# Kernel tuning notes

Measured on AMD Instinct MI355X. Metric: run time of the kernel, lower is better.

The kernel has to match this reference:

```python
import jax, jax.numpy as jnp
import numpy as np

# SLAYER neuron / simulation constants (from params)
THETA = 10.0      # spike threshold
TAU_SR = 10.0     # PSP (synaptic response) time constant
TS = 1.0          # simulation time step
TAU_RHO = 1.0     # surrogate-gradient width
SCALE_RHO = 1.0   # surrogate-gradient scale
ALPHA = float(np.exp(-TS / TAU_SR))  # leaky-filter decay per step

B, C_IN, T = 32, 156, 2048
HID, OUT = 512, 20


@jax.custom_vjp
def spike(u):
    # Hard threshold with SLAYER-style exponential surrogate gradient.
    return (u >= THETA).astype(u.dtype)

def _spike_fwd(u):
    return spike(u), u

def _spike_bwd(u, g):
    sg = (SCALE_RHO / TAU_RHO) * jnp.exp(-jnp.abs(u - THETA) / TAU_RHO)
    return (g * sg,)

spike.defvjp(_spike_fwd, _spike_bwd)


def psp(x):
    # Leaky exponential temporal filter along the LAST axis (SLAYER psp):
    # y[t] = ALPHA * y[t-1] + x[t]
    xt = jnp.moveaxis(x, -1, 0)  # [T, ...]
    def step(c, xi):
        c = ALPHA * c + xi
        return c, c
    _, y = jax.lax.scan(step, jnp.zeros_like(xt[0]), xt)
    return jnp.moveaxis(y, 0, -1)


def dense(x, W):
    # SLAYER dense layer: per-timestep fully-connected over channel dim.
    # x: [N, C, H, W, T], W: [O, C] -> [N, O, H, W, T]
    return jnp.einsum('oc,nchwt->nohwt', W, x)


def _make_perm():
    rng = np.random.default_rng(0)
    random_list = rng.permutation(np.arange(1, 40))
    perm = []
    for i in random_list:
        perm.append(2 * int(i) - 2)
        perm.append(2 * int(i) - 1)
    for i in random_list:
        perm.append(2 * int(i) - 2 + 78)
        perm.append(2 * int(i) - 1 + 78)
    return jnp.asarray(perm, dtype=jnp.int32)


def setup_inputs() -> dict:
    key = jax.random.key(0)
    k0, k1, k2, k3, k4 = jax.random.split(key, 5)
    spike_input = jax.random.randint(k0, (B, C_IN, 1, 1, T), 0, 2).astype(jnp.float32)
    W1 = jax.random.normal(k1, (HID, C_IN), dtype=jnp.float32) * (C_IN ** -0.5)
    W2 = jax.random.normal(k2, (OUT, HID), dtype=jnp.float32) * (HID ** -0.5)
    Wl1 = jax.random.normal(k3, (HID, T), dtype=jnp.float32) * (T ** -0.5)
    Wl2 = jax.random.normal(k4, (OUT, HID), dtype=jnp.float32) * (HID ** -0.5)
    perm = _make_perm()
    return {"spike_input": spike_input, "W1": W1, "W2": W2,
            "Wl1": Wl1, "Wl2": Wl2, "perm": perm}


def reference(spike_input, W1, W2, Wl1, Wl2, perm):
    # Branch 1: channel-dense over taxels, PSP + spike, twice.
    s1 = spike(psp(dense(spike_input, W1)))          # [B, HID, 1, 1, T]
    spike_output = spike(psp(dense(s1, W2)))         # [B, OUT, 1, 1, T]

    # Branch 2: transpose channel<->time, permute taxel axis, dense over time dim.
    x_t = jnp.swapaxes(spike_input, 1, 4)            # [B, T, 1, 1, C_IN]
    x_tp = x_t[..., perm]                            # gather on taxel axis
    l1 = spike(psp(dense(x_tp, Wl1)))                # [B, HID, 1, 1, C_IN]
    location_output = spike(psp(dense(l1, Wl2)))     # [B, OUT, 1, 1, C_IN]

    return jnp.concatenate([spike_output, location_output], axis=4)
```

## Files before the change

### kernel.cpp

```cpp
#include <hip/hip_runtime.h>

#define ALPHA  0.90483741803595952f
#define ALPHA8 0.44932896411722156f
#define THETA  10.0f
#define BF1    ((unsigned short)0x3F80)
#define ISCALE 0.015625f

typedef short   bf16x8 __attribute__((ext_vector_type(8)));
typedef float   f32x4  __attribute__((ext_vector_type(4)));
typedef float   f32x4v __attribute__((ext_vector_type(4)));
typedef unsigned short ushort4v __attribute__((ext_vector_type(4)));
typedef unsigned short ushort8v __attribute__((ext_vector_type(8)));
typedef unsigned char  uchar4v  __attribute__((ext_vector_type(4)));
typedef unsigned char  uchar8v  __attribute__((ext_vector_type(8)));
typedef long long i64;

#define DMA16(gsrc, ldst)                                                     \
    __builtin_amdgcn_global_load_lds(                                         \
        (const __attribute__((address_space(1))) unsigned int*)(gsrc),        \
        (__attribute__((address_space(3))) unsigned int*)(ldst), 16, 0, 0)

__device__ __forceinline__ unsigned short f2bf(float f) {
    unsigned int x = __float_as_uint(f);
    unsigned int r = (x + 0x7FFFu + ((x >> 16) & 1u)) >> 16;
    return (unsigned short)r;
}
__device__ __forceinline__ float bf2f(unsigned short h) {
    return __uint_as_float(((unsigned int)h) << 16);
}
__device__ __forceinline__ void split2(float w, unsigned short& h0,
                                       unsigned short& h1) {
    h0 = f2bf(w);          float r0 = w - bf2f(h0);
    h1 = f2bf(r0);
}
__device__ __forceinline__ unsigned char f2fp8(float f) {
    int pk = __builtin_amdgcn_cvt_pk_fp8_f32(f, 0.f, 0, false);
    return (unsigned char)(pk & 0xFF);
}
__device__ __forceinline__ float fp82f(unsigned char b) {
    return __builtin_amdgcn_cvt_f32_fp8((int)b, 0);
}

__global__ __launch_bounds__(256) void prep_scan_pack(
    const float* __restrict__ In, unsigned char* __restrict__ Infp8,
    unsigned short* __restrict__ Pbf,
    const float* __restrict__ W1,  const float* __restrict__ W2,
    const float* __restrict__ Wl1, const float* __restrict__ Wl2,
    unsigned short* __restrict__ W1p,  unsigned char* __restrict__ W2p8,
    unsigned char* __restrict__ Wl1p8, unsigned short* __restrict__ Wl2p)
{
    const int blk = blockIdx.x;
    if (blk >= 4992) {
        const int bidx = blk - 4992;
        if (bidx >= 512 && bidx < 544) {
            int m = bidx - 512;
            for (int k = threadIdx.x; k < 512; k += 256) {
                float w = (m < 20) ? W2[(long long)m * 512 + k] : 0.f;
                unsigned char h0 = f2fp8(w);
                unsigned char h1 = f2fp8(w - fp82f(h0));
                W2p8[(long long)m * 512 + k] = h0;
                W2p8[16384 + (long long)m * 512 + k] = h1;
            }
        } else if (bidx >= 544 && bidx < 1056) {
            int m = bidx - 544;
            for (int k = threadIdx.x; k < 2048; k += 256) {
                float w = Wl1[(long long)m * 2048 + k] * 64.0f;
                unsigned char h0 = f2fp8(w);
                unsigned char h1 = f2fp8(w - fp82f(h0));
                Wl1p8[(long long)m * 2048 + k] = h0;
                Wl1p8[1048576 + (long long)m * 2048 + k] = h1;
            }
        } else {
            const float* W; unsigned short* P; int M, K, Kp, Mp, m;
            if (bidx < 512) { W = W1;  P = W1p;  M = 512; K = 156; Kp = 160; Mp = 512; m = bidx; }
            else            { W = Wl2; P = Wl2p; M = 20;  K = 512; Kp = 512; Mp = 32;  m = bidx - 1056; }
            for (int k = threadIdx.x; k < Kp; k += 256) {
                float v = (m < M && k < K) ? W[(long long)m * K + k] : 0.f;
                unsigned short h0, h1;
                split2(v, h0, h1);
                P[(long long)m * Kp + k] = h0;
                P[(long long)Mp * Kp + (long long)m * Kp + k] = h1;
            }
        }
        return;
    }

    const int row = blk;
    const int tid = threadIdx.x;
    const float* x = In + (long long)row * 2048 + tid * 8;
    const unsigned char ONE8 = f2fp8(1.0f);

    float v[8];
    *(f32x4v*)&v[0] = *(const f32x4v*)x;
    *(f32x4v*)&v[4] = *(const f32x4v*)(x + 4);

    uchar8v raw;
    #pragma unroll
    for (int k = 0; k < 8; ++k) raw[k] = (v[k] >= 0.5f) ? ONE8 : (unsigned char)0;
    *(uchar8v*)(Infp8 + (long long)row * 2048 + tid * 8) = raw;

    float y = 0.f;
    #pragma unroll
    for (int k = 0; k < 8; ++k) { y = ALPHA * y + v[k]; v[k] = y; }

    __shared__ float sc[256];
    float val = y;
    sc[tid] = val;
    float m = ALPHA8;
    for (int d = 1; d < 256; d <<= 1) {
        __syncthreads();
        float p = (tid >= d) ? sc[tid - d] : 0.f;
        __syncthreads();
        val += m * p;
        sc[tid] = val;
        m *= m;
    }
    __syncthreads();
    float carry = (tid > 0) ? sc[tid - 1] : 0.f;

    ushort8v pv;
    float ak = ALPHA;
    #pragma unroll
    for (int k = 0; k < 8; ++k) {
        float yk = v[k] + ak * carry;
        ak *= ALPHA;
        pv[k] = f2bf(yk);
    }
    *(ushort8v*)(Pbf + (long long)row * 2048 + tid * 8) = pv;
}

__global__ __launch_bounds__(256) void transposeP(
    const unsigned short* __restrict__ Pbf, unsigned short* __restrict__ PT)
{
    __shared__ unsigned short Tile[64][72];
    const int t0 = blockIdx.x * 64;
    const int c0 = blockIdx.y * 64;
    const int b  = blockIdx.z;
    const int tid = threadIdx.x;

    #pragma unroll
    for (int s = 0; s < 2; ++s) {
        int id = tid + s * 256;
        int cc = id >> 3;
        int t8 = (id & 7) * 8;
        ushort8v v = {0,0,0,0,0,0,0,0};
        if (c0 + cc < 156)
            v = *(const ushort8v*)(Pbf + (long long)(b * 156 + c0 + cc) * 2048 + t0 + t8);
        *(ushort8v*)&Tile[cc][t8] = v;
    }
    __syncthreads();

    #pragma unroll
    for (int s = 0; s < 2; ++s) {
        int id = tid + s * 256;
        int t  = id >> 3;
        int c8 = (id & 7) * 8;
        if (c0 + c8 + 7 < 160) {
            unsigned short r[8];
            #pragma unroll
            for (int j = 0; j < 8; ++j) r[j] = Tile[c8 + j][t];
            *(ushort8v*)(PT + (long long)b * 327680 + (long long)(t0 + t) * 160 + c0 + c8)
                = *(ushort8v*)r;
        }
    }
}

__global__ __launch_bounds__(256) void mega_gemm1(
    const unsigned short* __restrict__ W1p,
    const unsigned short* __restrict__ PT,
    unsigned short* __restrict__ S1bits,
    const unsigned char* __restrict__ Wl1p8,
    const unsigned char* __restrict__ Infp8,
    unsigned short* __restrict__ Zp)
{
    __shared__ alignas(16) unsigned char SMEM[49152];
    const int bx  = blockIdx.x;
    const int tid = threadIdx.x;
    const int lane = tid & 63, w = tid >> 6;
    const int wy = w >> 1, wx = w & 1;
    const int l15 = lane & 15, kq = lane >> 4;
    const int key = (l15 >> 1) & 3;

    if (bx >= 1280) {
        unsigned char* Ab = SMEM;
        unsigned char* Bb = SMEM + 32768;

        const int id1 = bx - 1280;
        const int z  = id1 >> 6;
        const int m0 = ((id1 >> 4) & 3) * 128;
        const int n0 = (id1 & 15) * 128;
        const unsigned short* Tb = PT + (long long)z * 327680;

        auto dmaA = [&](int buf, int k0) {
            #pragma unroll
            for (int s = 0; s < 4; ++s) {
                int id = tid + s * 256;
                int pl = id >> 9, m = (id >> 2) & 127, g = id & 3;
                int gs = g ^ ((m >> 1) & 3);
                DMA16(W1p + (long long)pl * 81920 +
                      (long long)(m0 + m) * 160 + k0 + gs * 8,
                      Ab + buf * 16384 + id * 16);
            }
        };
        auto dmaB = [&](int buf, int k0) {
            #pragma unroll
            for (int s = 0; s < 2; ++s) {
                int id = tid + s * 256;
                int n = id >> 2, g = id & 3;
                int gs = g ^ ((n >> 1) & 3);
                DMA16(Tb + (long long)(n0 + n) * 160 + k0 + gs * 8,
                      Bb + buf * 8192 + id * 16);
            }
        };

        int aOff[2][4], bOff[4];
        #pragma unroll
        for (int pl = 0; pl < 2; ++pl)
            #pragma unroll
            for (int mt = 0; mt < 4; ++mt)
                aOff[pl][mt] = pl * 8192 + (wy * 64 + mt * 16 + l15) * 64 +
                               ((kq ^ key) * 16);
        #pragma unroll
        for (int nt = 0; nt < 4; ++nt)
            bOff[nt] = (wx * 64 + nt * 16 + l15) * 64 + ((kq ^ key) * 16);

        f32x4 acc[4][4] = {};

        dmaA(0, 0); dmaB(0, 0);
        __syncthreads();

        #pragma unroll
        for (int it = 0; it < 5; ++it) {
            const int cur = it & 1;
            if (it < 4) { dmaA(cur ^ 1, (it + 1) * 32); dmaB(cur ^ 1, (it + 1) * 32); }

            const unsigned char* Ac = Ab + cur * 16384;
            const unsigned char* Bc = Bb + cur * 8192;
            bf16x8 bfr[4];
            #pragma unroll
            for (int nt = 0; nt < 4; ++nt)
                bfr[nt] = *(const bf16x8*)(Bc + bOff[nt]);
            #pragma unroll
            for (int pl = 0; pl < 2; ++pl) {
                #pragma unroll
                for (int mt = 0; mt < 4; ++mt) {
                    bf16x8 afr = *(const bf16x8*)(Ac + aOff[pl][mt]);
                    #pragma unroll
                    for (int nt = 0; nt < 4; ++nt)
                        acc[mt][nt] = __builtin_amdgcn_mfma_f32_16x16x32_bf16(
                            afr, bfr[nt], acc[mt][nt], 0, 0, 0);
                }
            }
            __syncthreads();
        }

        unsigned short* Db = S1bits + (long long)z * 512 * 128;
        #pragma unroll
        for (int mt = 0; mt < 4; ++mt) {
            #pragma unroll
            for (int i = 0; i < 4; ++i) {
                int m = m0 + wy * 64 + mt * 16 + kq * 4 + i;
                #pragma unroll
                for (int nt = 0; nt < 4; ++nt) {
                    unsigned long long mask = __ballot(acc[mt][nt][i] >= THETA);
                    if (l15 == 0) {
                        int nchunk = (n0 + wx * 64 + nt * 16) >> 4;
                        Db[(long long)m * 128 + nchunk] =
                            (unsigned short)((mask >> (kq * 16)) & 0xFFFFu);
                    }
                }
            }
        }
    } else {
        unsigned char* Ab = SMEM;
        unsigned char* Bb = SMEM + 16384;

        const int id0 = bx;
        const int nIdx = id0 % 40;
        if (nIdx >= 39) return;
        const int rest = id0 / 40;
        const int n0  = nIdx * 128;
        const int m0  = (rest & 7) * 64;
        const int ksl = rest >> 3;
        const int ks0 = ksl * 512;

        auto dmaA8 = [&](int buf, int kk) {
            #pragma unroll
            for (int s = 0; s < 2; ++s) {
                int id = tid + s * 256;
                int pl = id >> 8, m = (id >> 2) & 63, g = id & 3;
                int gs = g ^ ((m >> 1) & 3);
                DMA16(Wl1p8 + (long long)pl * 1048576 +
                      (long long)(m0 + m) * 2048 + kk + gs * 16,
                      Ab + buf * 8192 + id * 16);
            }
        };
        auto dmaB8 = [&](int buf, int kk) {
            #pragma unroll
            for (int s = 0; s < 2; ++s) {
                int id = tid + s * 256;
                int n = id >> 2, g = id & 3;
                int gs = g ^ ((n >> 1) & 3);
                DMA16(Infp8 + (long long)(n0 + n) * 2048 + kk + gs * 16,
                      Bb + buf * 8192 + id * 16);
            }
        };

        int aO8[2][2][2], bO8[4][2];
        #pragma unroll
        for (int ks = 0; ks < 2; ++ks) {
            const int gl = ks * 2 + (kq >> 1);
            const int sub = ((gl ^ key) * 16) + (kq & 1) * 8;
            #pragma unroll
            for (int pl = 0; pl < 2; ++pl)
                #pragma unroll
                for (int mt = 0; mt < 2; ++mt)
                    aO8[pl][mt][ks] = pl * 4096 +
                        (wy * 32 + mt * 16 + l15) * 64 + sub;
            #pragma unroll
            for (int nt = 0; nt < 4; ++nt)
                bO8[nt][ks] = (wx * 64 + nt * 16 + l15) * 64 + sub;
        }

        f32x4 acc[2][4] = {};

        dmaA8(0, ks0); dmaB8(0, ks0);
        __syncthreads();

        #pragma unroll
        for (int it = 0; it < 8; ++it) {
            const int cur = it & 1;
            if (it < 7) { dmaA8(cur ^ 1, ks0 + (it + 1) * 64);
                          dmaB8(cur ^ 1, ks0 + (it + 1) * 64); }

            const unsigned char* Ac = Ab + cur * 8192;
            const unsigned char* Bc = Bb + cur * 8192;
            #pragma unroll
            for (int ks = 0; ks < 2; ++ks) {
                i64 bfr[4];
                #pragma unroll
                for (int nt = 0; nt < 4; ++nt)
                    bfr[nt] = *(const i64*)(Bc + bO8[nt][ks]);
                #pragma unroll
                for (int pl = 0; pl < 2; ++pl) {
                    #pragma unroll
                    for (int mt = 0; mt < 2; ++mt) {
                        i64 afr = *(const i64*)(Ac + aO8[pl][mt][ks]);
                        #pragma unroll
                        for (int nt = 0; nt < 4; ++nt)
                            acc[mt][nt] = __builtin_amdgcn_mfma_f32_16x16x32_fp8_fp8(
                                afr, bfr[nt], acc[mt][nt], 0, 0, 0);
                    }
                }
            }
            __syncthreads();
        }

        unsigned short* Tu = (unsigned short*)SMEM;
        #pragma unroll
        for (int mt = 0; mt < 2; ++mt) {
            #pragma unroll
            for (int i = 0; i < 4; ++i) {
                int mL = wy * 32 + mt * 16 + kq * 4 + i;
                #pragma unroll
                for (int nt = 0; nt < 4; ++nt) {
                    int nL = wx * 64 + nt * 16 + l15;
                    Tu[mL * 129 + nL] = f2bf(acc[mt][nt][i] * ISCALE);
                }
            }
        }
        __syncthreads();

        unsigned short* Zs = Zp + (long long)ksl * 2555904;
        #pragma unroll
        for (int s2 = 0; s2 < 32; ++s2) {
            int id = tid + s2 * 256;
            int cL = id >> 6;
            int mL = id & 63;
            int n = n0 + cL;
            int bb = n / 156, cc = n - bb * 156;
            Zs[(long long)cc * 16384 + bb * 512 + m0 + mL] = Tu[mL * 129 + cL];
        }
    }
}

__global__ __launch_bounds__(256) void mega_stage2(
    const unsigned char* __restrict__ W2p8,
    const unsigned short* __restrict__ S1bits,
    float* __restrict__ C2p,
    const unsigned short* __restrict__ Zp,
    const int* __restrict__ perm,
    unsigned short* __restrict__ L1T)
{
    __shared__ alignas(16) unsigned char SMEM[20608];
    const int bx  = blockIdx.x;
    const int tid = threadIdx.x;

    if (bx < 1024) {
        auto As = (unsigned char (*)[32][72])SMEM;
        auto Bs = (unsigned char (*)[72])(SMEM + 4608);

        const int lane = tid & 63, w = tid >> 6;
        const int l15 = lane & 15, kq = lane >> 4;
        const int n0  = (bx & 15) * 128;
        const int ksl = (bx >> 4) & 1;
        const int b   = bx >> 5;
        const int ks0 = ksl * 256;

        const unsigned short* Bb = S1bits + (long long)b * 512 * 128;
        const unsigned char ONE8 = f2fp8(1.0f);

        int aPl[2], aM[2], aK8[2];
        #pragma unroll
        for (int s = 0; s < 2; ++s) {
            int id = tid + s * 256;
            aPl[s] = id >> 8; int rem = id & 255;
            aM[s] = rem >> 3; aK8[s] = (rem & 7) * 8;
        }
        const int kb = (tid >> 4) * 4;
        const int nb = (tid & 15) * 8;
        const int nchunk = (n0 + nb) >> 4;
        const int nshift = nb & 15;

        f32x4 acc[2][2] = {};
        uchar8v aReg[2];
        unsigned short bBits[4];

        auto loadA = [&](int k0) {
            #pragma unroll
            for (int s = 0; s < 2; ++s)
                aReg[s] = *(const uchar8v*)(W2p8 + (long long)aPl[s] * 16384 +
                                            (long long)aM[s] * 512 + k0 + aK8[s]);
        };
        auto loadB = [&](int k0) {
            #pragma unroll
            for (int kk2 = 0; kk2 < 4; ++kk2)
                bBits[kk2] = Bb[(long long)(k0 + kb + kk2) * 128 + nchunk];
        };
        auto stage = [&]() {
            #pragma unroll
            for (int s = 0; s < 2; ++s) *(uchar8v*)&As[aPl[s]][aM[s]][aK8[s]] = aReg[s];
            unsigned char bv[4][8];
            #pragma unroll
            for (int kk2 = 0; kk2 < 4; ++kk2) {
                unsigned int bits = ((unsigned int)bBits[kk2] >> nshift) & 0xFFu;
                #pragma unroll
                for (int j = 0; j < 8; ++j)
                    bv[kk2][j] = ((bits >> j) & 1u) ? ONE8 : (unsigned char)0;
            }
            #pragma unroll
            for (int j = 0; j < 8; ++j) {
                uchar4v v4 = { bv[0][j], bv[1][j], bv[2][j], bv[3][j] };
                *(uchar4v*)&Bs[nb + j][kb] = v4;
            }
        };

        loadA(ks0); loadB(ks0);
        stage();
        __syncthreads();

        #pragma unroll
        for (int it = 0; it < 4; ++it) {
            const int kn = ks0 + (it + 1) * 64;
            if (it < 3) { loadA(kn); loadB(kn); }

            #pragma unroll
            for (int ks = 0; ks < 2; ++ks) {
                i64 bfr[2];
                #pragma unroll
                for (int nt = 0; nt < 2; ++nt)
                    bfr[nt] = *(const i64*)&Bs[w * 32 + nt * 16 + l15][ks * 32 + kq * 8];
                #pragma unroll
                for (int s = 0; s < 2; ++s) {
                    #pragma unroll
                    for (int mt = 0; mt < 2; ++mt) {
                        i64 afr = *(const i64*)&As[s][mt * 16 + l15][ks * 32 + kq * 8];
                        #pragma unroll
                        for (int nt = 0; nt < 2; ++nt)
                            acc[mt][nt] = __builtin_amdgcn_mfma_f32_16x16x32_fp8_fp8(
                                afr, bfr[nt], acc[mt][nt], 0, 0, 0);
                    }
                }
            }
            __syncthreads();
            if (it < 3) {
                stage();
                __syncthreads();
            }
        }

        float* Cb = C2p + (long long)b * 20 * 2048 + (long long)ksl * 1310720LL;
        #pragma unroll
        for (int mt = 0; mt < 2; ++mt) {
            #pragma unroll
            for (int i = 0; i < 4; ++i) {
                int m = mt * 16 + kq * 4 + i;
                if (m >= 20) continue;
                #pragma unroll
                for (int nt = 0; nt < 2; ++nt) {
                    int n = n0 + w * 32 + nt * 16 + l15;
                    Cb[(long long)m * 2048 + n] = acc[mt][nt][i];
                }
            }
        }
    } else {
        auto Xs = (float (*)[32])SMEM;
        int* p  = (int*)(SMEM + 19968);

        const int r0 = (bx - 1024) * 32;
        for (int i = tid; i < 156; i += 256) p[i] = perm[i];

        const int row = tid & 31;
        const int cq  = tid >> 5;
        #pragma unroll
        for (int it = 0; it < 20; ++it) {
            int c = it * 8 + cq;
            if (c < 156) {
                long long base = (long long)c * 16384 + r0 + row;
                float s = bf2f(Zp[base]) + bf2f(Zp[base + 2555904]) +
                          bf2f(Zp[base + 2 * 2555904]) + bf2f(Zp[base + 3 * 2555904]);
                Xs[c][row] = s;
            }
        }
        __syncthreads();

        if (tid < 32) {
            float y = 0.f;
            for (int c = 0; c < 156; ++c) {
                y = ALPHA * y + Xs[p[c]][tid];
                L1T[(long long)c * 16384 + r0 + tid] = (y >= THETA) ? BF1 : 0;
            }
        }
    }
}

__global__ __launch_bounds__(256) void mega_stage3(
    const float* __restrict__ C2p, float* __restrict__ out,
    const unsigned short* __restrict__ Wl2p,
    const unsigned short* __restrict__ L1T)
{
    __shared__ alignas(16) unsigned char SMEM[36864];
    const int bx  = blockIdx.x;
    const int tid = threadIdx.x;

    if (bx < 640) {
        float* sc = (float*)SMEM;
        const int row = bx;
        const float* x = C2p + (long long)row * 2048 + tid * 8;

        float v[8];
        #pragma unroll
        for (int k = 0; k < 8; ++k) v[k] = x[k] + x[k + 1310720LL];

        float y = 0.f;
        #pragma unroll
        for (int k = 0; k < 8; ++k) { y = ALPHA * y + v[k]; v[k] = y; }

        float val = y;
        sc[tid] = val;
        float m = ALPHA8;
        for (int d = 1; d < 256; d <<= 1) {
            __syncthreads();
            float p = (tid >= d) ? sc[tid - d] : 0.f;
            __syncthreads();
            val += m * p;
            sc[tid] = val;
            m *= m;
        }
        __syncthreads();
        float carry = (tid > 0) ? sc[tid - 1] : 0.f;

        float* o = out + (long long)row * 2204 + tid * 8;
        float ak = ALPHA;
        #pragma unroll
        for (int k = 0; k < 8; ++k) {
            float yk = v[k] + ak * carry;
            ak *= ALPHA;
            o[k] = (yk >= THETA) ? 1.0f : 0.0f;
        }
    } else {
        auto As = (unsigned short (*)[32][72])SMEM;
        auto Bs = (unsigned short (*)[72])(SMEM + 9216);

        const int b  = bx - 640;
        const int lane = tid & 63, w = tid >> 6;
        const int l15 = lane & 15, kq = lane >> 4;

        f32x4 acc[2][3] = {};

        for (int k0 = 0; k0 < 512; k0 += 64) {
            #pragma unroll
            for (int s = 0; s < 2; ++s) {
                int id = tid + s * 256;
                int pl = id >> 8, rem = id & 255;
                int m = rem >> 3, k8 = (rem & 7) * 8;
                ushort8v v = *(const ushort8v*)(Wl2p + (long long)pl * 16384 +
                                                (long long)m * 512 + k0 + k8);
                *(ushort8v*)&As[pl][m][k8] = v;
            }
            #pragma unroll
            for (int s = 0; s < 6; ++s) {
                int id = tid + s * 256;
                int n = id >> 3, k8 = (id & 7) * 8;
                ushort8v v = {0,0,0,0,0,0,0,0};
                if (n < 156)
                    v = *(const ushort8v*)(L1T + (long long)n * 16384 +
                                           b * 512 + k0 + k8);
                *(ushort8v*)&Bs[n][k8] = v;
            }
            __syncthreads();

            #pragma unroll
            for (int ks = 0; ks < 2; ++ks) {
                bf16x8 bfr[3];
                #pragma unroll
                for (int nt = 0; nt < 3; ++nt)
                    bfr[nt] = *(const bf16x8*)&Bs[w * 48 + nt * 16 + l15][ks * 32 + kq * 8];
                #pragma unroll
                for (int s = 0; s < 2; ++s) {
                    #pragma unroll
                    for (int mt = 0; mt < 2; ++mt) {
                        bf16x8 afr = *(const bf16x8*)&As[s][mt * 16 + l15][ks * 32 + kq * 8];
                        #pragma unroll
                        for (int nt = 0; nt < 3; ++nt)
                            acc[mt][nt] = __builtin_amdgcn_mfma_f32_16x16x32_bf16(
                                afr, bfr[nt], acc[mt][nt], 0, 0, 0);
                    }
                }
            }
            __syncthreads();
        }

        float* Cs = (float*)SMEM;
        #pragma unroll
        for (int mt = 0; mt < 2; ++mt) {
            #pragma unroll
            for (int i = 0; i < 4; ++i) {
                int m = mt * 16 + kq * 4 + i;
                #pragma unroll
                for (int nt = 0; nt < 3; ++nt) {
                    int n = w * 48 + nt * 16 + l15;
                    Cs[m * 193 + n] = acc[mt][nt][i];
                }
            }
        }
        __syncthreads();

        if (tid < 20) {
            const float* cr = Cs + tid * 193;
            float* o = out + (long long)(b * 20 + tid) * 2204 + 2048;
            float y = 0.f;
            for (int c = 0; c < 156; ++c) {
                y = ALPHA * y + cr[c];
                o[c] = (y >= THETA) ? 1.0f : 0.0f;
            }
        }
    }
}

extern "C" void kernel_launch(void* const* d_in, const int* in_sizes, int n_in,
                              void* d_out, int out_size, void* d_ws, size_t ws_size,
                              hipStream_t stream)
{
    const float* In  = (const float*)d_in[0];
    const float* W1  = (const float*)d_in[1];
    const float* W2  = (const float*)d_in[2];
    const float* Wl1 = (const float*)d_in[3];
    const float* Wl2 = (const float*)d_in[4];
    const int*  perm = (const int*)d_in[5];
    float* out = (float*)d_out;

    float* ws = (float*)d_ws;
    unsigned short* S1bits = (unsigned short*)ws;
    float* C2p = ws + 1048576LL;
    unsigned char*  Infp8 = (unsigned char*)(ws + 3670016LL);
    unsigned short* Pbf  = (unsigned short*)(ws + 6225920LL);
    unsigned short* PT   = (unsigned short*)(ws + 11337728LL);
    unsigned short* W1p  = (unsigned short*)(ws + 16580608LL);
    unsigned char*  W2p8 = (unsigned char*)(ws + 16662528LL);
    unsigned char*  Wl1p8= (unsigned char*)(ws + 16670720LL);
    unsigned short* Wl2p = (unsigned short*)(ws + 17195008LL);
    unsigned short* Zpbf = (unsigned short*)(ws + 17211392LL);
    unsigned short* L1T  = (unsigned short*)(ws + 22323200LL);

    dim3 blk(256);

    prep_scan_pack<<<dim3(6080), blk, 0, stream>>>(
        In, Infp8, Pbf, W1, W2, Wl1, Wl2, W1p, W2p8, Wl1p8, Wl2p);
    transposeP<<<dim3(32, 3, 32), blk, 0, stream>>>(Pbf, PT);

    mega_gemm1<<<dim3(3328), blk, 0, stream>>>(W1p, PT, S1bits,
                                               Wl1p8, Infp8, Zpbf);
    mega_stage2<<<dim3(1536), blk, 0, stream>>>(W2p8, S1bits, C2p,
                                                Zpbf, perm, L1T);
    mega_stage3<<<dim3(672), blk, 0, stream>>>(C2p, out, Wl2p, L1T);

    (void)in_sizes; (void)n_in; (void)out_size; (void)ws_size;
}
```

Before: 187.0 us.

## Use warp-shuffle scans, transpose spike bitmask layout, double-buffer fp8 GEMM, reorder blocks

The block-wide PSP prefix scans in prep and stage3 move from a 256-step shared-memory scan with two barriers per step to a 64-lane shuffle scan plus a small cross-wave combine. The S1 spike bitmask is stored column-major so the consumer can fetch four chunks with one 64-bit load. The stage2 fp8 GEMM gains LDS double buffering so only one barrier is needed per iteration. The LDS tile pitch changes from 129 to 130, and block index ranges are reordered so heavy or weight-prep blocks launch first. The cost is more LDS per block and the risk that the hard-coded decay constants in the combine step lose precision.

```diff
diff --git a/kernel.cpp b/kernel.cpp
--- a/kernel.cpp
+++ b/kernel.cpp
@@ -2,6 +2,7 @@
 
 #define ALPHA  0.90483741803595952f
 #define ALPHA8 0.44932896411722156f
+#define A64C   5.82e-23f
 #define THETA  10.0f
 #define BF1    ((unsigned short)0x3F80)
 #define ISCALE 0.015625f
@@ -50,43 +51,49 @@
     unsigned char* __restrict__ Wl1p8, unsigned short* __restrict__ Wl2p)
 {
     const int blk = blockIdx.x;
-    if (blk >= 4992) {
-        const int bidx = blk - 4992;
-        if (bidx >= 512 && bidx < 544) {
-            int m = bidx - 512;
-            for (int k = threadIdx.x; k < 512; k += 256) {
+    const int tid = threadIdx.x;
+    if (blk < 1088) {
+        if (blk < 512) {
+            int m = blk;
+            for (int k = tid; k < 2048; k += 256) {
+                float w = Wl1[(long long)m * 2048 + k] * 64.0f;
+                unsigned char h0 = f2fp8(w);
+                unsigned char h1 = f2fp8(w - fp82f(h0));
+                Wl1p8[(long long)m * 2048 + k] = h0;
+                Wl1p8[1048576 + (long long)m * 2048 + k] = h1;
+            }
+        } else if (blk < 1024) {
+            int m = blk - 512;
+            for (int k = tid; k < 160; k += 256) {
+                float v = (k < 156) ? W1[(long long)m * 156 + k] : 0.f;
+                unsigned short h0, h1;
+                split2(v, h0, h1);
+                W1p[(long long)m * 160 + k] = h0;
+                W1p[81920 + (long long)m * 160 + k] = h1;
+            }
+        } else if (blk < 1056) {
+            int m = blk - 1024;
+            for (int k = tid; k < 512; k += 256) {
                 float w = (m < 20) ? W2[(long long)m * 512 + k] : 0.f;
                 unsigned char h0 = f2fp8(w);
                 unsigned char h1 = f2fp8(w - fp82f(h0));
                 W2p8[(long long)m * 512 + k] = h0;
                 W2p8[16384 + (long long)m * 512 + k] = h1;
             }
-        } else if (bidx >= 544 && bidx < 1056) {
-            int m = bidx - 544;
-            for (int k = threadIdx.x; k < 2048; k += 256) {
-                float w = Wl1[(long long)m * 2048 + k] * 64.0f;
-                unsigned char h0 = f2fp8(w);
-                unsigned char h1 = f2fp8(w - fp82f(h0));
-                Wl1p8[(long long)m * 2048 + k] = h0;
-                Wl1p8[1048576 + (long long)m * 2048 + k] = h1;
-            }
         } else {
-            const float* W; unsigned short* P; int M, K, Kp, Mp, m;
-            if (bidx < 512) { W = W1;  P = W1p;  M = 512; K = 156; Kp = 160; Mp = 512; m = bidx; }
-            else            { W = Wl2; P = Wl2p; M = 20;  K = 512; Kp = 512; Mp = 32;  m = bidx - 1056; }
-            for (int k = threadIdx.x; k < Kp; k += 256) {
-                float v = (m < M && k < K) ? W[(long long)m * K + k] : 0.f;
+            int m = blk - 1056;
+            for (int k = tid; k < 512; k += 256) {
+                float v = (m < 20) ? Wl2[(long long)m * 512 + k] : 0.f;
                 unsigned short h0, h1;
                 split2(v, h0, h1);
-                P[(long long)m * Kp + k] = h0;
-                P[(long long)Mp * Kp + (long long)m * Kp + k] = h1;
+                Wl2p[(long long)m * 512 + k] = h0;
+                Wl2p[16384 + (long long)m * 512 + k] = h1;
             }
         }
         return;
     }
 
-    const int row = blk;
-    const int tid = threadIdx.x;
+    const int row = blk - 1088;
     const float* x = In + (long long)row * 2048 + tid * 8;
     const unsigned char ONE8 = f2fp8(1.0f);
 
@@ -103,20 +110,24 @@
     #pragma unroll
     for (int k = 0; k < 8; ++k) { y = ALPHA * y + v[k]; v[k] = y; }
 
-    __shared__ float sc[256];
-    float val = y;
-    sc[tid] = val;
-    float m = ALPHA8;
-    for (int d = 1; d < 256; d <<= 1) {
-        __syncthreads();
-        float p = (tid >= d) ? sc[tid - d] : 0.f;
-        __syncthreads();
-        val += m * p;
-        sc[tid] = val;
-        m *= m;
+    const int lane = tid & 63, wid = tid >> 6;
+    float val = y, mm = ALPHA8;
+    #pragma unroll
+    for (int d = 1; d < 64; d <<= 1) {
+        float p = __shfl_up(val, d);
+        if (lane >= d) val += mm * p;
+        mm *= mm;
     }
+    __shared__ float wsum[4];
+    if (lane == 63) wsum[wid] = val;
     __syncthreads();
-    float carry = (tid > 0) ? sc[tid - 1] : 0.f;
+    float pw = 0.f;
+    #pragma unroll
+    for (int w2 = 0; w2 < 3; ++w2)
+        if (w2 < wid) pw = pw * A64C + wsum[w2];
+    float prev = __shfl_up(val, 1);
+    float a8l  = __expf(-0.8f * (float)lane);
+    float carry = (lane == 0) ? pw : (prev + a8l * pw);
 
     ushort8v pv;
     float ak = ALPHA;
@@ -265,7 +276,7 @@
                     unsigned long long mask = __ballot(acc[mt][nt][i] >= THETA);
                     if (l15 == 0) {
                         int nchunk = (n0 + wx * 64 + nt * 16) >> 4;
-                        Db[(long long)m * 128 + nchunk] =
+                        Db[(long long)nchunk * 512 + m] =
                             (unsigned short)((mask >> (kq * 16)) & 0xFFFFu);
                     }
                 }
@@ -365,7 +376,7 @@
                 #pragma unroll
                 for (int nt = 0; nt < 4; ++nt) {
                     int nL = wx * 64 + nt * 16 + l15;
-                    Tu[mL * 129 + nL] = f2bf(acc[mt][nt][i] * ISCALE);
+                    Tu[mL * 130 + nL] = f2bf(acc[mt][nt][i] * ISCALE);
                 }
             }
         }
@@ -379,7 +390,7 @@
             int mL = id & 63;
             int n = n0 + cL;
             int bb = n / 156, cc = n - bb * 156;
-            Zs[(long long)cc * 16384 + bb * 512 + m0 + mL] = Tu[mL * 129 + cL];
+            Zs[(long long)cc * 16384 + bb * 512 + m0 + mL] = Tu[mL * 130 + cL];
         }
     }
 }
@@ -392,19 +403,20 @@
     const int* __restrict__ perm,
     unsigned short* __restrict__ L1T)
 {
-    __shared__ alignas(16) unsigned char SMEM[20608];
+    __shared__ alignas(16) unsigned char SMEM[27648];
     const int bx  = blockIdx.x;
     const int tid = threadIdx.x;
 
-    if (bx < 1024) {
-        auto As = (unsigned char (*)[32][72])SMEM;
-        auto Bs = (unsigned char (*)[72])(SMEM + 4608);
-
+    if (bx >= 512) {
+        auto As = (unsigned char (*)[2][32][72])SMEM;
+        auto Bs = (unsigned char (*)[128][72])(SMEM + 9216);
+
+        const int bxg = bx - 512;
         const int lane = tid & 63, w = tid >> 6;
         const int l15 = lane & 15, kq = lane >> 4;
-        const int n0  = (bx & 15) * 128;
-        const int ksl = (bx >> 4) & 1;
-        const int b   = bx >> 5;
+        const int n0  = (bxg & 15) * 128;
+        const int ksl = (bxg >> 4) & 1;
+        const int b   = bxg >> 5;
         const int ks0 = ksl * 256;
 
         const unsigned short* Bb = S1bits + (long long)b * 512 * 128;
@@ -433,13 +445,16 @@
                                             (long long)aM[s] * 512 + k0 + aK8[s]);
         };
         auto loadB = [&](int k0) {
-            #pragma unroll
-            for (int kk2 = 0; kk2 < 4; ++kk2)
-                bBits[kk2] = Bb[(long long)(k0 + kb + kk2) * 128 + nchunk];
+            unsigned long long u = *(const unsigned long long*)
+                (Bb + (long long)nchunk * 512 + k0 + kb);
+            bBits[0] = (unsigned short)u;
+            bBits[1] = (unsigned short)(u >> 16);
+            bBits[2] = (unsigned short)(u >> 32);
+            bBits[3] = (unsigned short)(u >> 48);
         };
-        auto stage = [&]() {
-            #pragma unroll
-            for (int s = 0; s < 2; ++s) *(uchar8v*)&As[aPl[s]][aM[s]][aK8[s]] = aReg[s];
+        auto stage = [&](int buf) {
+            #pragma unroll
+            for (int s = 0; s < 2; ++s) *(uchar8v*)&As[buf][aPl[s]][aM[s]][aK8[s]] = aReg[s];
             unsigned char bv[4][8];
             #pragma unroll
             for (int kk2 = 0; kk2 < 4; ++kk2) {
@@ -451,16 +466,17 @@
             #pragma unroll
             for (int j = 0; j < 8; ++j) {
                 uchar4v v4 = { bv[0][j], bv[1][j], bv[2][j], bv[3][j] };
-                *(uchar4v*)&Bs[nb + j][kb] = v4;
+                *(uchar4v*)&Bs[buf][nb + j][kb] = v4;
             }
         };
 
         loadA(ks0); loadB(ks0);
-        stage();
+        stage(0);
         __syncthreads();
 
         #pragma unroll
         for (int it = 0; it < 4; ++it) {
+            const int cur = it & 1;
             const int kn = ks0 + (it + 1) * 64;
             if (it < 3) { loadA(kn); loadB(kn); }
 
@@ -469,12 +485,12 @@
                 i64 bfr[2];
                 #pragma unroll
                 for (int nt = 0; nt < 2; ++nt)
-                    bfr[nt] = *(const i64*)&Bs[w * 32 + nt * 16 + l15][ks * 32 + kq * 8];
-                #pragma unroll
-                for (int s = 0; s < 2; ++s) {
+                    bfr[nt] = *(const i64*)&Bs[cur][w * 32 + nt * 16 + l15][ks * 32 + kq * 8];
+                #pragma unroll
+                for (int pl = 0; pl < 2; ++pl) {
                     #pragma unroll
                     for (int mt = 0; mt < 2; ++mt) {
-                        i64 afr = *(const i64*)&As[s][mt * 16 + l15][ks * 32 + kq * 8];
+                        i64 afr = *(const i64*)&As[cur][pl][mt * 16 + l15][ks * 32 + kq * 8];
                         #pragma unroll
                         for (int nt = 0; nt < 2; ++nt)
                             acc[mt][nt] = __builtin_amdgcn_mfma_f32_16x16x32_fp8_fp8(
@@ -482,11 +498,9 @@
                     }
                 }
             }
+
+            if (it < 3) stage(cur ^ 1);
             __syncthreads();
-            if (it < 3) {
-                stage();
-                __syncthreads();
-            }
         }
 
         float* Cb = C2p + (long long)b * 20 * 2048 + (long long)ksl * 1310720LL;
@@ -507,7 +521,7 @@
         auto Xs = (float (*)[32])SMEM;
         int* p  = (int*)(SMEM + 19968);
 
-        const int r0 = (bx - 1024) * 32;
+        const int r0 = bx * 32;
         for (int i = tid; i < 156; i += 256) p[i] = perm[i];
 
         const int row = tid & 31;
@@ -543,9 +557,8 @@
     const int bx  = blockIdx.x;
     const int tid = threadIdx.x;
 
-    if (bx < 640) {
-        float* sc = (float*)SMEM;
-        const int row = bx;
+    if (bx >= 32) {
+        const int row = bx - 32;
         const float* x = C2p + (long long)row * 2048 + tid * 8;
 
         float v[8];
@@ -556,19 +569,24 @@
         #pragma unroll
         for (int k = 0; k < 8; ++k) { y = ALPHA * y + v[k]; v[k] = y; }
 
-        float val = y;
-        sc[tid] = val;
-        float m = ALPHA8;
-        for (int d = 1; d < 256; d <<= 1) {
-            __syncthreads();
-            float p = (tid >= d) ? sc[tid - d] : 0.f;
-            __syncthreads();
-            val += m * p;
-            sc[tid] = val;
-            m *= m;
-        }
+        const int lane = tid & 63, wid = tid >> 6;
+        float val = y, mm = ALPHA8;
+        #pragma unroll
+        for (int d = 1; d < 64; d <<= 1) {
+            float p = __shfl_up(val, d);
+            if (lane >= d) val += mm * p;
+            mm *= mm;
+        }
+        float* wsum = (float*)SMEM;
+        if (lane == 63) wsum[wid] = val;
         __syncthreads();
-        float carry = (tid > 0) ? sc[tid - 1] : 0.f;
+        float pw = 0.f;
+        #pragma unroll
+        for (int w2 = 0; w2 < 3; ++w2)
+            if (w2 < wid) pw = pw * A64C + wsum[w2];
+        float prev = __shfl_up(val, 1);
+        float a8l  = __expf(-0.8f * (float)lane);
+        float carry = (lane == 0) ? pw : (prev + a8l * pw);
 
         float* o = out + (long long)row * 2204 + tid * 8;
         float ak = ALPHA;
@@ -582,7 +600,7 @@
         auto As = (unsigned short (*)[32][72])SMEM;
         auto Bs = (unsigned short (*)[72])(SMEM + 9216);
 
-        const int b  = bx - 640;
+        const int b  = bx;
         const int lane = tid & 63, w = tid >> 6;
         const int l15 = lane & 15, kq = lane >> 4;
 
```

Measured after the change: 178.7 us. 4.4% less time.
